# Kernel tuning notes

Measured on AMD Instinct MI355X. Metric: run time of the kernel, lower is better.

Reference implementation:

```python
import jax, jax.numpy as jnp
import numpy as np

B, T, INP, HID, ACT = 64, 1000, 64, 512, 2

def setup_inputs() -> dict:
    key = jax.random.key(0)
    k1, k2, k3, k4, k5 = jax.random.split(key, 5)
    s_hh = (6.0 / (HID + HID)) ** 0.5  # xavier_uniform bounds
    s_ih = (6.0 / (INP + HID)) ** 0.5
    s_fc = (6.0 / (HID + ACT)) ** 0.5
    return {
        "inp": jax.random.normal(k1, (B, T, INP), dtype=jnp.float32),
        "hn": jax.random.normal(k2, (1, B, HID), dtype=jnp.float32),
        "W_hh": jax.random.uniform(k3, (HID, HID), jnp.float32, -s_hh, s_hh),
        "W_ih": jax.random.uniform(k4, (INP, HID), jnp.float32, -s_ih, s_ih),
        "W_fc": jax.random.uniform(k5, (HID, ACT), jnp.float32, -s_fc, s_fc),
        "b_fc": jnp.zeros((ACT,), dtype=jnp.float32),
    }

def reference(inp, hn, W_hh, W_ih, W_fc, b_fc):
    # Precompute input projections for all timesteps in one big GEMM: [B,T,H]
    inp_proj = jnp.einsum("bti,ih->bth", inp, W_ih)
    h0 = hn[0]  # [B, H]

    def step(h, x_t):
        h_next = jax.nn.sigmoid(h @ W_hh + x_t)
        return h_next, h_next

    # scan over time: xs must be time-major
    _, hs = jax.lax.scan(step, h0, jnp.swapaxes(inp_proj, 0, 1))
    rnn_out = jnp.swapaxes(hs, 0, 1)  # [B, T, H]
    hn_last = rnn_out[:, -1, :][None]  # [1, B, H]
    out = jax.nn.sigmoid(rnn_out @ W_fc + b_fc)  # [B, T, ACT]
    return (out, hn_last, rnn_out)
```

## Files before the change

### kernel.cpp

```cpp
#include <hip/hip_runtime.h>
#include <hip/hip_bf16.h>
#include <stdint.h>
#include <math.h>

#define B   64
#define T   1000
#define INP 64
#define HID 512
#define ACT 2

#define NSLICE 4
#define MROWS  2
#define NGROUP (B / MROWS)
#define NBLOCKS (NGROUP * NSLICE)
#define NLAUNCH 256
#define WORK_PER_XCD 16
#define COLS   (HID / NSLICE)
#define HLPAD  544

#define FAST_GUARD 256

typedef __attribute__((ext_vector_type(8))) short short8;
typedef __attribute__((ext_vector_type(4))) float floatx4;

__device__ __forceinline__ uint64_t l2_load64(const uint64_t* p) {
  uint64_t v;
  asm volatile("global_load_dwordx2 %0, %1, off sc0\n\t"
               "s_waitcnt vmcnt(0)"
               : "=v"(v) : "v"(p) : "memory");
  return v;
}
__device__ __forceinline__ void l2_store64(uint64_t* p, uint64_t v) {
  asm volatile("global_store_dwordx2 %0, %1, off"
               :: "v"(p), "v"(v) : "memory");
}
__device__ __forceinline__ int get_xcc_id() {
  int x;
  asm volatile("s_getreg_b32 %0, hwreg(HW_REG_XCC_ID)" : "=s"(x));
  return x & 7;
}

#define CTRL_WORDS 16

__global__ __launch_bounds__(256) void init_kernel(
    const float* __restrict__ hn, uint64_t* __restrict__ h_fast,
    uint64_t* __restrict__ h_safe, uint32_t* __restrict__ ctrl) {
  if (blockIdx.x == 0 && threadIdx.x < CTRL_WORDS) ctrl[threadIdx.x] = 0;
  const int i   = blockIdx.x * 256 + threadIdx.x;
  const int g   = i >> 9;
  const int col = i & (HID - 1);
  __hip_bfloat16 b0 = __float2bfloat16(hn[(2 * g) * HID + col]);
  __hip_bfloat16 b1 = __float2bfloat16(hn[(2 * g + 1) * HID + col]);
  const uint32_t w0 = ((uint32_t)*reinterpret_cast<unsigned short*>(&b0)) << 16;
  const uint32_t w1 = ((uint32_t)*reinterpret_cast<unsigned short*>(&b1)) << 16;
  const uint64_t v  = (uint64_t)w0 | ((uint64_t)w1 << 32);
  const size_t p1 = (size_t)NGROUP * HID + i;
  h_fast[p1] = v;
  h_safe[p1] = v;
  h_fast[i] = 0x0000FFFE0000FFFEull;
  h_safe[i] = 0x0000FFFE0000FFFEull;
}

__global__ __launch_bounds__(256) void xproj_kernel(
    const float* __restrict__ inp, const float* __restrict__ W_ih,
    float* __restrict__ rnn) {
  __shared__ float xin[16 * INP];
  const int tid = threadIdx.x;
  const long r0 = (long)blockIdx.x * 16;

  const float4* inp4 = (const float4*)(inp + r0 * INP);
  ((float4*)xin)[tid] = inp4[tid];
  __syncthreads();

  const int j = tid, j2 = tid + 256;
  float acc0[16], acc1[16];
#pragma unroll
  for (int r = 0; r < 16; ++r) { acc0[r] = 0.f; acc1[r] = 0.f; }

  for (int i = 0; i < INP; ++i) {
    const float w0 = W_ih[i * HID + j];
    const float w1 = W_ih[i * HID + j2];
#pragma unroll
    for (int r = 0; r < 16; ++r) {
      const float x = xin[r * INP + i];
      acc0[r] = fmaf(x, w0, acc0[r]);
      acc1[r] = fmaf(x, w1, acc1[r]);
    }
  }
#pragma unroll
  for (int r = 0; r < 16; ++r) {
    rnn[(r0 + r) * HID + j]  = acc0[r];
    rnn[(r0 + r) * HID + j2] = acc1[r];
  }
}

__global__ __launch_bounds__(512) void rnn_mfma(
    const float* __restrict__ W_hh, float* __restrict__ rnn,
    float* __restrict__ hn_out, uint64_t* __restrict__ h_fast,
    uint64_t* __restrict__ h_safe, uint32_t* __restrict__ ctrl) {
  __shared__ __align__(16) unsigned short hl[2][MROWS][HLPAD];
  __shared__ int sh_g, sh_s, sh_work, sh_mode;

  const int tid  = threadIdx.x;

  if (tid == 0) {
    uint32_t* cnt      = ctrl;
    uint32_t* claimed  = ctrl + 8;
    uint32_t* arrivals = ctrl + 9;
    uint32_t* flag     = ctrl + 10;
    const int xcc = get_xcc_id();
    const int slot = (int)__hip_atomic_fetch_add(
        &cnt[xcc], 1u, __ATOMIC_RELAXED, __HIP_MEMORY_SCOPE_AGENT);
    int work = 0, g = 0, s = 0;
    if (slot < WORK_PER_XCD) {
      g = xcc * 4 + (slot >> 2);
      s = slot & 3;
      work = 1;
      __hip_atomic_fetch_add(claimed, 1u, __ATOMIC_RELEASE,
                             __HIP_MEMORY_SCOPE_AGENT);
    }
    const int arr = (int)__hip_atomic_fetch_add(
        arrivals, 1u, __ATOMIC_ACQ_REL, __HIP_MEMORY_SCOPE_AGENT);
    if (arr == NLAUNCH - 1) {
      const uint32_t c = __hip_atomic_load(claimed, __ATOMIC_ACQUIRE,
                                           __HIP_MEMORY_SCOPE_AGENT);
      __hip_atomic_store(flag, (c == NBLOCKS) ? 2u : 1u, __ATOMIC_RELEASE,
                         __HIP_MEMORY_SCOPE_AGENT);
    }
    uint32_t f = 0; int guard = 0;
    do {
      f = __hip_atomic_load(flag, __ATOMIC_ACQUIRE, __HIP_MEMORY_SCOPE_AGENT);
    } while (f == 0 && ++guard < (1 << 20));
    if (f != 2) {
      work = (blockIdx.x < NBLOCKS);
      g = blockIdx.x & (NGROUP - 1);
      s = blockIdx.x >> 5;
    }
    sh_g = g; sh_s = s; sh_work = work; sh_mode = (f == 2);
  }
  __syncthreads();
  if (!sh_work) return;

  const int g = __builtin_amdgcn_readfirstlane(sh_g);
  const int s = __builtin_amdgcn_readfirstlane(sh_s);
  int fastmode = __builtin_amdgcn_readfirstlane(sh_mode);

  const int lane = tid & 63;
  const int w    = tid >> 6;
  const int r0   = g * MROWS;
  const int n_base = s * COLS + w * 16;

  const int lm = lane & 15;
  const int lq = lane >> 4;
  const int cc = n_base + lm;

  short8 bfrag[16];
#pragma unroll
  for (int kt = 0; kt < 16; ++kt) {
    short8 f;
#pragma unroll
    for (int i = 0; i < 8; ++i) {
      const int k = kt * 32 + lq * 8 + i;
      __hip_bfloat16 hb = __float2bfloat16(W_hh[k * HID + cc]);
      f[i] = *reinterpret_cast<short*>(&hb);
    }
    bfrag[kt] = f;
  }

  const int  arow   = lm & 1;
  const bool remote = ((tid >> 7) != s);
  const bool prod   = (lq == 0);

  long ro0 = ((long)r0 * T + 0) * HID + cc;
  long ro1 = ((long)(r0 + 1) * T + 0) * HID + cc;
  float xp0 = 0.f, xp1 = 0.f;
  if (prod) { xp0 = rnn[ro0]; xp1 = rnn[ro1]; }

  for (int t = 0; t < T; ++t) {
    const int p = (t + 1) & 1;

    if (t == 0 || remote) {
      const size_t idx = ((size_t)p * NGROUP + g) * HID + tid;
      const uint64_t want = (uint64_t)(t & 0xFFFF) * 0x0000000100000001ull;
      uint64_t v = 0;
      if (fastmode) {
        int ok = 0;
        for (int it = 0; it < FAST_GUARD; ++it) {
          v = l2_load64(h_fast + idx);
          if (((v ^ want) & 0x0000FFFF0000FFFFull) == 0) { ok = 1; break; }
        }
        if (!ok) fastmode = 0;
      }
      if (!fastmode) {
        int guard = 0;
        for (;;) {
          v = __hip_atomic_load(h_safe + idx, __ATOMIC_RELAXED,
                                __HIP_MEMORY_SCOPE_AGENT);
          if (((v ^ want) & 0x0000FFFF0000FFFFull) == 0) break;
          if (++guard > (1 << 20)) break;
        }
      }
      hl[p][0][tid] = (unsigned short)((uint32_t)v >> 16);
      hl[p][1][tid] = (unsigned short)((uint32_t)(v >> 32) >> 16);
    }
    __syncthreads();

    float nxp0 = 0.f, nxp1 = 0.f;
    long nro0 = ro0, nro1 = ro1;
    if (prod && t + 1 < T) {
      nro0 = ro0 + HID; nro1 = ro1 + HID;
      nxp0 = rnn[nro0]; nxp1 = rnn[nro1];
    }

    floatx4 c0 = {0.f, 0.f, 0.f, 0.f}, c1 = c0, c2 = c0, c3 = c0;
    const unsigned short* ap = &hl[p][arow][lq * 8];
#pragma unroll
    for (int kt = 0; kt < 16; kt += 4) {
      short8 a0 = *(const short8*)(ap + (kt + 0) * 32);
      short8 a1 = *(const short8*)(ap + (kt + 1) * 32);
      short8 a2 = *(const short8*)(ap + (kt + 2) * 32);
      short8 a3 = *(const short8*)(ap + (kt + 3) * 32);
      c0 = __builtin_amdgcn_mfma_f32_16x16x32_bf16(a0, bfrag[kt + 0], c0, 0, 0, 0);
      c1 = __builtin_amdgcn_mfma_f32_16x16x32_bf16(a1, bfrag[kt + 1], c1, 0, 0, 0);
      c2 = __builtin_amdgcn_mfma_f32_16x16x32_bf16(a2, bfrag[kt + 2], c2, 0, 0, 0);
      c3 = __builtin_amdgcn_mfma_f32_16x16x32_bf16(a3, bfrag[kt + 3], c3, 0, 0, 0);
    }

    if (prod) {
      const float z0 = c0[0] + c1[0] + c2[0] + c3[0] + xp0;
      const float z1 = c0[1] + c1[1] + c2[1] + c3[1] + xp1;
      const float h0 = 1.f / (1.f + __expf(-z0));
      const float h1 = 1.f / (1.f + __expf(-z1));
      __hip_bfloat16 b0 = __float2bfloat16(h0);
      __hip_bfloat16 b1 = __float2bfloat16(h1);
      const unsigned short u0 = *reinterpret_cast<unsigned short*>(&b0);
      const unsigned short u1 = *reinterpret_cast<unsigned short*>(&b1);

      const uint32_t tag = (uint32_t)(t + 1) & 0xFFFFu;
      const uint64_t word =
          (uint64_t)(((uint32_t)u0 << 16) | tag) |
          ((uint64_t)(((uint32_t)u1 << 16) | tag) << 32);
      const size_t didx = ((size_t)(t & 1) * NGROUP + g) * HID + cc;
      l2_store64(h_fast + didx, word);
      __hip_atomic_store(h_safe + didx, word, __ATOMIC_RELAXED,
                         __HIP_MEMORY_SCOPE_AGENT);

      hl[t & 1][0][cc] = u0;
      hl[t & 1][1][cc] = u1;

      rnn[ro0] = h0;
      rnn[ro1] = h1;
      if (t == T - 1) {
        hn_out[r0 * HID + cc]       = h0;
        hn_out[(r0 + 1) * HID + cc] = h1;
      }
      xp0 = nxp0; xp1 = nxp1; ro0 = nro0; ro1 = nro1;
    }
  }
}

__global__ __launch_bounds__(256) void fc_kernel(
    const float* __restrict__ rnn, const float* __restrict__ W_fc,
    const float* __restrict__ b_fc, float* __restrict__ out) {
  const int lane = threadIdx.x & 63;
  const int wid  = threadIdx.x >> 6;
  const long row = (long)blockIdx.x * 4 + wid;

  const float4* __restrict__ hrow = (const float4*)(rnn + row * HID);
  const float4* __restrict__ Wfc4 = (const float4*)W_fc;

  float a0 = 0.f, a1 = 0.f;
#pragma unroll
  for (int u = 0; u < 2; ++u) {
    const float4 hv = hrow[lane * 2 + u];
    const int j0 = lane * 8 + u * 4;
    const float4 wA = Wfc4[(j0 >> 1)];
    const float4 wB = Wfc4[(j0 >> 1) + 1];
    a0 += hv.x * wA.x + hv.y * wA.z + hv.z * wB.x + hv.w * wB.z;
    a1 += hv.x * wA.y + hv.y * wA.w + hv.z * wB.y + hv.w * wB.w;
  }
#pragma unroll
  for (int off = 32; off > 0; off >>= 1) {
    a0 += __shfl_down(a0, off, 64);
    a1 += __shfl_down(a1, off, 64);
  }
  if (lane == 0) {
    out[row * 2 + 0] = 1.f / (1.f + __expf(-(a0 + b_fc[0])));
    out[row * 2 + 1] = 1.f / (1.f + __expf(-(a1 + b_fc[1])));
  }
}

extern "C" void kernel_launch(void* const* d_in, const int* in_sizes, int n_in,
                              void* d_out, int out_size, void* d_ws,
                              size_t ws_size, hipStream_t stream) {
  const float* inp  = (const float*)d_in[0];
  const float* hn   = (const float*)d_in[1];
  const float* W_hh = (const float*)d_in[2];
  const float* W_ih = (const float*)d_in[3];
  const float* W_fc = (const float*)d_in[4];
  const float* b_fc = (const float*)d_in[5];

  float* out    = (float*)d_out;
  float* hn_out = out + (long)B * T * ACT;
  float* rnn    = hn_out + (long)B * HID;

  uint32_t* ctrl   = (uint32_t*)d_ws;
  uint64_t* h_fast = (uint64_t*)((char*)d_ws + 256);
  const size_t HCNT = (size_t)2 * NGROUP * HID;
  uint64_t* h_safe =
      (ws_size >= 256 + 2 * HCNT * sizeof(uint64_t)) ? (h_fast + HCNT)
                                                     : h_fast;

  hipLaunchKernelGGL(init_kernel, dim3((NGROUP * HID) / 256), dim3(256), 0,
                     stream, hn, h_fast, h_safe, ctrl);
  hipLaunchKernelGGL(xproj_kernel, dim3((B * T) / 16), dim3(256), 0, stream,
                     inp, W_ih, rnn);
  hipLaunchKernelGGL(rnn_mfma, dim3(NLAUNCH), dim3(512), 0, stream,
                     W_hh, rnn, hn_out, h_fast, h_safe, ctrl);
  hipLaunchKernelGGL(fc_kernel, dim3((B * T) / 4), dim3(256), 0, stream,
                     rnn, W_fc, b_fc, out);
}
```

Baseline: 1.497 ms.

## Batch input-projection loads and hidden-state stores in 16-step LDS chunks

Instead of one global load of the next step's input projection and one global store of h on every timestep, each wave now prefetches 16 timesteps of projections into registers, drops them into LDS at chunk boundaries, and stages outputs in LDS to flush every 16 steps. This takes per-step global memory traffic off the serial recurrence critical path. In exchange it uses more LDS and adds a burst of work every 16 steps plus a tail flush. The staging relies on the existing per-step barrier for ordering, so correctness depends on identifiers like w, lane and n_base matching the column mapping.

```diff
diff --git a/kernel.cpp b/kernel.cpp
--- a/kernel.cpp
+++ b/kernel.cpp
@@ -99,6 +99,8 @@
     float* __restrict__ hn_out, uint64_t* __restrict__ h_fast,
     uint64_t* __restrict__ h_safe, uint32_t* __restrict__ ctrl) {
   __shared__ __align__(16) unsigned short hl[2][MROWS][HLPAD];
+  __shared__ float xbuf[8][16][2][16];
+  __shared__ float rstage[16][2][COLS];
   __shared__ int sh_g, sh_s, sh_work, sh_mode;
 
   const int tid  = threadIdx.x;
@@ -171,13 +173,17 @@
   const bool remote = ((tid >> 7) != s);
   const bool prod   = (lq == 0);
 
-  long ro0 = ((long)r0 * T + 0) * HID + cc;
-  long ro1 = ((long)(r0 + 1) * T + 0) * HID + cc;
-  float xp0 = 0.f, xp1 = 0.f;
-  if (prod) { xp0 = rnn[ro0]; xp1 = rnn[ro1]; }
+  float xreg[8];
+#pragma unroll
+  for (int i = 0; i < 8; ++i) {
+    const int v = i * 64 + lane;
+    const int st = v >> 5, row = (v >> 4) & 1, c = v & 15;
+    xreg[i] = rnn[((long)(r0 + row) * T + st) * HID + n_base + c];
+  }
 
   for (int t = 0; t < T; ++t) {
-    const int p = (t + 1) & 1;
+    const int p  = (t + 1) & 1;
+    const int tb = t & 15;
 
     if (t == 0 || remote) {
       const size_t idx = ((size_t)p * NGROUP + g) * HID + tid;
@@ -203,14 +209,30 @@
       hl[p][0][tid] = (unsigned short)((uint32_t)v >> 16);
       hl[p][1][tid] = (unsigned short)((uint32_t)(v >> 32) >> 16);
     }
+
+    if (tb == 0) {
+#pragma unroll
+      for (int i = 0; i < 8; ++i) {
+        const int v = i * 64 + lane;
+        xbuf[w][v >> 5][(v >> 4) & 1][v & 15] = xreg[i];
+      }
+      if (t > 0 && prod) {
+        const int tf = t - 16;
+        for (int u = 0; u < 16; ++u) {
+          rnn[((long)r0 * T + (tf + u)) * HID + cc]       = rstage[u][0][w * 16 + lm];
+          rnn[((long)(r0 + 1) * T + (tf + u)) * HID + cc] = rstage[u][1][w * 16 + lm];
+        }
+      }
+#pragma unroll
+      for (int i = 0; i < 8; ++i) {
+        const int v = i * 64 + lane;
+        const int st = v >> 5, row = (v >> 4) & 1, c = v & 15;
+        const int tt = t + 16 + st;
+        if (tt < T)
+          xreg[i] = rnn[((long)(r0 + row) * T + tt) * HID + n_base + c];
+      }
+    }
     __syncthreads();
-
-    float nxp0 = 0.f, nxp1 = 0.f;
-    long nro0 = ro0, nro1 = ro1;
-    if (prod && t + 1 < T) {
-      nro0 = ro0 + HID; nro1 = ro1 + HID;
-      nxp0 = rnn[nro0]; nxp1 = rnn[nro1];
-    }
 
     floatx4 c0 = {0.f, 0.f, 0.f, 0.f}, c1 = c0, c2 = c0, c3 = c0;
     const unsigned short* ap = &hl[p][arow][lq * 8];
@@ -227,6 +249,8 @@
     }
 
     if (prod) {
+      const float xp0 = xbuf[w][tb][0][lm];
+      const float xp1 = xbuf[w][tb][1][lm];
       const float z0 = c0[0] + c1[0] + c2[0] + c3[0] + xp0;
       const float z1 = c0[1] + c1[1] + c2[1] + c3[1] + xp1;
       const float h0 = 1.f / (1.f + __expf(-z0));
@@ -248,13 +272,20 @@
       hl[t & 1][0][cc] = u0;
       hl[t & 1][1][cc] = u1;
 
-      rnn[ro0] = h0;
-      rnn[ro1] = h1;
+      rstage[tb][0][w * 16 + lm] = h0;
+      rstage[tb][1][w * 16 + lm] = h1;
       if (t == T - 1) {
         hn_out[r0 * HID + cc]       = h0;
         hn_out[(r0 + 1) * HID + cc] = h1;
       }
-      xp0 = nxp0; xp1 = nxp1; ro0 = nro0; ro1 = nro1;
+    }
+  }
+
+  if (prod) {
+    const int tf = (T - 1) & ~15;
+    for (int u = 0; u < T - tf; ++u) {
+      rnn[((long)r0 * T + (tf + u)) * HID + cc]       = rstage[u][0][w * 16 + lm];
+      rnn[((long)(r0 + 1) * T + (tf + u)) * HID + cc] = rstage[u][1][w * 16 + lm];
     }
   }
 }
```

New measurement: 1.555 ms. 3.9% more time.

## Halve RNN block to 4 waves, each computing two 16-column MFMA tiles

Applied to the files above, without the earlier changes.

Each workgroup of the recurrent kernel now uses 256 threads (4 waves) instead of 512. Each wave owns 32 output columns, using two sets of W_hh fragments and interleaved MFMA chains that share the A operand. The remote hidden-state exchange is widened to 128-bit loads, each covering two tagged words, so fewer threads poll per step. The aim is to cut barrier and polling overhead per timestep. In exchange, register pressure doubles (two 16-fragment weight arrays) and each wave does twice the serial MFMA work.

```diff
diff --git a/kernel.cpp b/kernel.cpp
--- a/kernel.cpp
+++ b/kernel.cpp
@@ -16,16 +16,19 @@
 #define NLAUNCH 256
 #define WORK_PER_XCD 16
 #define COLS   (HID / NSLICE)
+#define NWAVES 4
 #define HLPAD  544
 
 #define FAST_GUARD 256
+#define SAFE_GUARD (1 << 18)
 
 typedef __attribute__((ext_vector_type(8))) short short8;
 typedef __attribute__((ext_vector_type(4))) float floatx4;
-
-__device__ __forceinline__ uint64_t l2_load64(const uint64_t* p) {
-  uint64_t v;
-  asm volatile("global_load_dwordx2 %0, %1, off sc0\n\t"
+typedef __attribute__((ext_vector_type(4))) uint32_t uint32x4;
+
+__device__ __forceinline__ uint32x4 l2_load128(const void* p) {
+  uint32x4 v;
+  asm volatile("global_load_dwordx4 %0, %1, off sc0\n\t"
                "s_waitcnt vmcnt(0)"
                : "=v"(v) : "v"(p) : "memory");
   return v;
@@ -94,7 +97,7 @@
   }
 }
 
-__global__ __launch_bounds__(512) void rnn_mfma(
+__global__ __launch_bounds__(256, 1) void rnn_mfma(
     const float* __restrict__ W_hh, float* __restrict__ rnn,
     float* __restrict__ hn_out, uint64_t* __restrict__ h_fast,
     uint64_t* __restrict__ h_safe, uint32_t* __restrict__ ctrl) {
@@ -148,71 +151,88 @@
   const int lane = tid & 63;
   const int w    = tid >> 6;
   const int r0   = g * MROWS;
-  const int n_base = s * COLS + w * 16;
+  const int n_base = s * COLS + w * 32;
 
   const int lm = lane & 15;
   const int lq = lane >> 4;
-  const int cc = n_base + lm;
-
-  short8 bfrag[16];
+  const int cca = n_base + lm;
+  const int ccb = cca + 16;
+
+  short8 bfA[16], bfB[16];
 #pragma unroll
   for (int kt = 0; kt < 16; ++kt) {
-    short8 f;
+    short8 fa, fb;
 #pragma unroll
     for (int i = 0; i < 8; ++i) {
       const int k = kt * 32 + lq * 8 + i;
-      __hip_bfloat16 hb = __float2bfloat16(W_hh[k * HID + cc]);
-      f[i] = *reinterpret_cast<short*>(&hb);
-    }
-    bfrag[kt] = f;
+      __hip_bfloat16 ha = __float2bfloat16(W_hh[k * HID + cca]);
+      __hip_bfloat16 hb = __float2bfloat16(W_hh[k * HID + ccb]);
+      fa[i] = *reinterpret_cast<short*>(&ha);
+      fb[i] = *reinterpret_cast<short*>(&hb);
+    }
+    bfA[kt] = fa;
+    bfB[kt] = fb;
   }
 
   const int  arow   = lm & 1;
-  const bool remote = ((tid >> 7) != s);
+  const bool remote = (w != s);
   const bool prod   = (lq == 0);
 
-  long ro0 = ((long)r0 * T + 0) * HID + cc;
-  long ro1 = ((long)(r0 + 1) * T + 0) * HID + cc;
-  float xp0 = 0.f, xp1 = 0.f;
-  if (prod) { xp0 = rnn[ro0]; xp1 = rnn[ro1]; }
+  long roa0 = ((long)r0 * T) * HID + cca;
+  long roa1 = ((long)(r0 + 1) * T) * HID + cca;
+  long rob0 = roa0 + 16, rob1 = roa1 + 16;
+  float xpa0 = 0.f, xpa1 = 0.f, xpb0 = 0.f, xpb1 = 0.f;
+  if (prod) {
+    xpa0 = rnn[roa0]; xpa1 = rnn[roa1];
+    xpb0 = rnn[rob0]; xpb1 = rnn[rob1];
+  }
 
   for (int t = 0; t < T; ++t) {
     const int p = (t + 1) & 1;
 
     if (t == 0 || remote) {
-      const size_t idx = ((size_t)p * NGROUP + g) * HID + tid;
-      const uint64_t want = (uint64_t)(t & 0xFFFF) * 0x0000000100000001ull;
-      uint64_t v = 0;
+      const size_t idx = ((size_t)p * NGROUP + g) * HID + 2 * tid;
+      const uint32_t want = (uint32_t)t & 0xFFFFu;
+      uint32x4 v = {0, 0, 0, 0};
       if (fastmode) {
         int ok = 0;
         for (int it = 0; it < FAST_GUARD; ++it) {
-          v = l2_load64(h_fast + idx);
-          if (((v ^ want) & 0x0000FFFF0000FFFFull) == 0) { ok = 1; break; }
+          v = l2_load128(h_fast + idx);
+          if ((((v[0] ^ want) | (v[1] ^ want) | (v[2] ^ want) |
+                (v[3] ^ want)) & 0xFFFFu) == 0) { ok = 1; break; }
         }
         if (!ok) fastmode = 0;
       }
       if (!fastmode) {
         int guard = 0;
         for (;;) {
-          v = __hip_atomic_load(h_safe + idx, __ATOMIC_RELAXED,
-                                __HIP_MEMORY_SCOPE_AGENT);
-          if (((v ^ want) & 0x0000FFFF0000FFFFull) == 0) break;
-          if (++guard > (1 << 20)) break;
+          const uint64_t a = __hip_atomic_load(h_safe + idx, __ATOMIC_RELAXED,
+                                               __HIP_MEMORY_SCOPE_AGENT);
+          const uint64_t b = __hip_atomic_load(h_safe + idx + 1,
+                                               __ATOMIC_RELAXED,
+                                               __HIP_MEMORY_SCOPE_AGENT);
+          v[0] = (uint32_t)a; v[1] = (uint32_t)(a >> 32);
+          v[2] = (uint32_t)b; v[3] = (uint32_t)(b >> 32);
+          if ((((v[0] ^ want) | (v[1] ^ want) | (v[2] ^ want) |
+                (v[3] ^ want)) & 0xFFFFu) == 0) break;
+          if (++guard > SAFE_GUARD) break;
         }
       }
-      hl[p][0][tid] = (unsigned short)((uint32_t)v >> 16);
-      hl[p][1][tid] = (unsigned short)((uint32_t)(v >> 32) >> 16);
+      *reinterpret_cast<uint32_t*>(&hl[p][0][2 * tid]) =
+          (v[0] >> 16) | (v[2] & 0xFFFF0000u);
+      *reinterpret_cast<uint32_t*>(&hl[p][1][2 * tid]) =
+          (v[1] >> 16) | (v[3] & 0xFFFF0000u);
     }
     __syncthreads();
 
-    float nxp0 = 0.f, nxp1 = 0.f;
-    long nro0 = ro0, nro1 = ro1;
+    float na0 = 0.f, na1 = 0.f, nb0 = 0.f, nb1 = 0.f;
     if (prod && t + 1 < T) {
-      nro0 = ro0 + HID; nro1 = ro1 + HID;
-      nxp0 = rnn[nro0]; nxp1 = rnn[nro1];
-    }
-
-    floatx4 c0 = {0.f, 0.f, 0.f, 0.f}, c1 = c0, c2 = c0, c3 = c0;
+      na0 = rnn[roa0 + HID]; na1 = rnn[roa1 + HID];
+      nb0 = rnn[rob0 + HID]; nb1 = rnn[rob1 + HID];
+    }
+
+    floatx4 c0a = {0.f, 0.f, 0.f, 0.f}, c1a = c0a, c2a = c0a, c3a = c0a;
+    floatx4 c0b = c0a, c1b = c0a, c2b = c0a, c3b = c0a;
     const unsigned short* ap = &hl[p][arow][lq * 8];
 #pragma unroll
     for (int kt = 0; kt < 16; kt += 4) {
@@ -220,41 +240,64 @@
       short8 a1 = *(const short8*)(ap + (kt + 1) * 32);
       short8 a2 = *(const short8*)(ap + (kt + 2) * 32);
       short8 a3 = *(const short8*)(ap + (kt + 3) * 32);
-      c0 = __builtin_amdgcn_mfma_f32_16x16x32_bf16(a0, bfrag[kt + 0], c0, 0, 0, 0);
-      c1 = __builtin_amdgcn_mfma_f32_16x16x32_bf16(a1, bfrag[kt + 1], c1, 0, 0, 0);
-      c2 = __builtin_amdgcn_mfma_f32_16x16x32_bf16(a2, bfrag[kt + 2], c2, 0, 0, 0);
-      c3 = __builtin_amdgcn_mfma_f32_16x16x32_bf16(a3, bfrag[kt + 3], c3, 0, 0, 0);
+      c0a = __builtin_amdgcn_mfma_f32_16x16x32_bf16(a0, bfA[kt + 0], c0a, 0, 0, 0);
+      c0b = __builtin_amdgcn_mfma_f32_16x16x32_bf16(a0, bfB[kt + 0], c0b, 0, 0, 0);
+      c1a = __builtin_amdgcn_mfma_f32_16x16x32_bf16(a1, bfA[kt + 1], c1a, 0, 0, 0);
+      c1b = __builtin_amdgcn_mfma_f32_16x16x32_bf16(a1, bfB[kt + 1], c1b, 0, 0, 0);
+      c2a = __builtin_amdgcn_mfma_f32_16x16x32_bf16(a2, bfA[kt + 2], c2a, 0, 0, 0);
+      c2b = __builtin_amdgcn_mfma_f32_16x16x32_bf16(a2, bfB[kt + 2], c2b, 0, 0, 0);
+      c3a = __builtin_amdgcn_mfma_f32_16x16x32_bf16(a3, bfA[kt + 3], c3a, 0, 0, 0);
+      c3b = __builtin_amdgcn_mfma_f32_16x16x32_bf16(a3, bfB[kt + 3], c3b, 0, 0, 0);
     }
 
     if (prod) {
-      const float z0 = c0[0] + c1[0] + c2[0] + c3[0] + xp0;
-      const float z1 = c0[1] + c1[1] + c2[1] + c3[1] + xp1;
-      const float h0 = 1.f / (1.f + __expf(-z0));
-      const float h1 = 1.f / (1.f + __expf(-z1));
-      __hip_bfloat16 b0 = __float2bfloat16(h0);
-      __hip_bfloat16 b1 = __float2bfloat16(h1);
-      const unsigned short u0 = *reinterpret_cast<unsigned short*>(&b0);
-      const unsigned short u1 = *reinterpret_cast<unsigned short*>(&b1);
+      const float za0 = (c0a[0] + c1a[0]) + (c2a[0] + c3a[0]) + xpa0;
+      const float za1 = (c0a[1] + c1a[1]) + (c2a[1] + c3a[1]) + xpa1;
+      const float zb0 = (c0b[0] + c1b[0]) + (c2b[0] + c3b[0]) + xpb0;
+      const float zb1 = (c0b[1] + c1b[1]) + (c2b[1] + c3b[1]) + xpb1;
+      const float ha0 = 1.f / (1.f + __expf(-za0));
+      const float ha1 = 1.f / (1.f + __expf(-za1));
+      const float hb0 = 1.f / (1.f + __expf(-zb0));
+      const float hb1 = 1.f / (1.f + __expf(-zb1));
+      __hip_bfloat16 ba0 = __float2bfloat16(ha0);
+      __hip_bfloat16 ba1 = __float2bfloat16(ha1);
+      __hip_bfloat16 bb0 = __float2bfloat16(hb0);
+      __hip_bfloat16 bb1 = __float2bfloat16(hb1);
+      const unsigned short ua0 = *reinterpret_cast<unsigned short*>(&ba0);
+      const unsigned short ua1 = *reinterpret_cast<unsigned short*>(&ba1);
+      const unsigned short ub0 = *reinterpret_cast<unsigned short*>(&bb0);
+      const unsigned short ub1 = *reinterpret_cast<unsigned short*>(&bb1);
 
       const uint32_t tag = (uint32_t)(t + 1) & 0xFFFFu;
-      const uint64_t word =
-          (uint64_t)(((uint32_t)u0 << 16) | tag) |
-          ((uint64_t)(((uint32_t)u1 << 16) | tag) << 32);
-      const size_t didx = ((size_t)(t & 1) * NGROUP + g) * HID + cc;
-      l2_store64(h_fast + didx, word);
-      __hip_atomic_store(h_safe + didx, word, __ATOMIC_RELAXED,
+      const uint64_t worda =
+          (uint64_t)(((uint32_t)ua0 << 16) | tag) |
+          ((uint64_t)(((uint32_t)ua1 << 16) | tag) << 32);
+      const uint64_t wordb =
+          (uint64_t)(((uint32_t)ub0 << 16) | tag) |
+          ((uint64_t)(((uint32_t)ub1 << 16) | tag) << 32);
+      const size_t dbase = ((size_t)(t & 1) * NGROUP + g) * HID;
+      l2_store64(h_fast + dbase + cca, worda);
+      l2_store64(h_fast + dbase + ccb, wordb);
+      __hip_atomic_store(h_safe + dbase + cca, worda, __ATOMIC_RELAXED,
                          __HIP_MEMORY_SCOPE_AGENT);
-
-      hl[t & 1][0][cc] = u0;
-      hl[t & 1][1][cc] = u1;
-
-      rnn[ro0] = h0;
-      rnn[ro1] = h1;
+      __hip_atomic_store(h_safe + dbase + ccb, wordb, __ATOMIC_RELAXED,
+                         __HIP_MEMORY_SCOPE_AGENT);
+
+      hl[t & 1][0][cca] = ua0;
+      hl[t & 1][1][cca] = ua1;
+      hl[t & 1][0][ccb] = ub0;
+      hl[t & 1][1][ccb] = ub1;
+
+      rnn[roa0] = ha0; rnn[roa1] = ha1;
+      rnn[rob0] = hb0; rnn[rob1] = hb1;
       if (t == T - 1) {
-        hn_out[r0 * HID + cc]       = h0;
-        hn_out[(r0 + 1) * HID + cc] = h1;
+        hn_out[r0 * HID + cca]       = ha0;
+        hn_out[(r0 + 1) * HID + cca] = ha1;
+        hn_out[r0 * HID + ccb]       = hb0;
+        hn_out[(r0 + 1) * HID + ccb] = hb1;
       }
-      xp0 = nxp0; xp1 = nxp1; ro0 = nro0; ro1 = nro1;
+      xpa0 = na0; xpa1 = na1; xpb0 = nb0; xpb1 = nb1;
+      roa0 += HID; roa1 += HID; rob0 += HID; rob1 += HID;
     }
   }
 }
@@ -315,7 +358,7 @@
                      stream, hn, h_fast, h_safe, ctrl);
   hipLaunchKernelGGL(xproj_kernel, dim3((B * T) / 16), dim3(256), 0, stream,
                      inp, W_ih, rnn);
-  hipLaunchKernelGGL(rnn_mfma, dim3(NLAUNCH), dim3(512), 0, stream,
+  hipLaunchKernelGGL(rnn_mfma, dim3(NLAUNCH), dim3(256), 0, stream,
                      W_hh, rnn, hn_out, h_fast, h_safe, ctrl);
   hipLaunchKernelGGL(fc_kernel, dim3((B * T) / 4), dim3(256), 0, stream,
                      rnn, W_fc, b_fc, out);
```

After: 1.779 ms. 18.8% more time.
